# Kernel tuning notes

Hardware: AMD Instinct MI355X
Metric: run time of the kernel (lower is better)

## Reference

```python
import jax, jax.numpy as jnp
import numpy as np

B, T, C, H = 4, 4096, 512, 64

def setup_inputs() -> dict:
    key = jax.random.key(0)
    ks = jax.random.split(key, 9)
    k = jax.random.normal(ks[0], (B, T, C), dtype=jnp.float32)
    v = jax.random.normal(ks[1], (B, T, C), dtype=jnp.float32)
    q = jax.random.normal(ks[2], (B, T, C), dtype=jnp.float32)
    # causal lower-triangular mask, positions with 0 are masked to -inf
    mask = jnp.tril(jnp.ones((T, T), dtype=jnp.int32))
    s = 1.0 / np.sqrt(C)
    kW = jax.random.normal(ks[3], (C, H), dtype=jnp.float32) * s
    kb = jax.random.normal(ks[4], (H,), dtype=jnp.float32) * s
    vW = jax.random.normal(ks[5], (C, H), dtype=jnp.float32) * s
    vb = jax.random.normal(ks[6], (H,), dtype=jnp.float32) * s
    qW = jax.random.normal(ks[7], (C, H), dtype=jnp.float32) * s
    qb = jax.random.normal(ks[8], (H,), dtype=jnp.float32) * s
    return {"k": k, "v": v, "q": q, "mask": mask,
            "kW": kW, "kb": kb, "vW": vW, "vb": vb, "qW": qW, "qb": qb}

def reference(k, v, q, mask, kW, kb, vW, vb, qW, qb):
    C_in = k.shape[-1]
    kp = k @ kW + kb                              # [B,T,H]
    qp = q @ qW + qb                              # [B,T,H]
    # NOTE: original scales by embedding_size**-0.5 (C), not head_size**-0.5
    attn = jnp.einsum('bth,bsh->bts', qp, kp) * (C_in ** -0.5)  # [B,T,T]
    attn = jnp.where(mask[None, :, :] == 0, -jnp.inf, attn)
    attn = jax.nn.softmax(attn, axis=-1)
    vp = v @ vW + vb                              # [B,T,H]
    out = attn @ vp                               # [B,T,H]
    return out
```

## Files before the change

### kernel.cpp

```cpp
#include <hip/hip_runtime.h>
#include <hip/hip_bf16.h>

#define Bq 4
#define Tq 4096
#define Cq 512
#define Hq 64
#define NCH 8
#define CT 16
#define NEG_BIG (-3.0e38f)

using bf16   = __bf16;
using bf16x8 = __attribute__((ext_vector_type(8))) __bf16;
using bf16x4 = __attribute__((ext_vector_type(4))) __bf16;
using f32x4  = __attribute__((ext_vector_type(4))) float;
using f32x16 = __attribute__((ext_vector_type(16))) float;

static __device__ __forceinline__ float other_half_f(float x) {
    return __shfl_xor(x, 32, 64);
}
static __device__ __forceinline__ unsigned other_half_u(unsigned x) {
    return (unsigned)__shfl_xor((int)x, 32, 64);
}
static __device__ __forceinline__ unsigned pk2(float x, float y) {
    union { bf16 h[2]; unsigned u; } t;
    t.h[0] = (bf16)x; t.h[1] = (bf16)y;
    return t.u;
}
union W8 { unsigned u[4]; bf16x8 v; };

__global__ __launch_bounds__(256) void prep_weights_kernel(
    const float* __restrict__ kW, const float* __restrict__ qW,
    const float* __restrict__ vW, bf16* __restrict__ WT)
{
    int i = blockIdx.x * 256 + threadIdx.x;
    int t = i >> 15;
    int r = i & 32767;
    int h = r >> 9;
    int c = r & 511;
    const float* W = (t == 0) ? kW : (t == 1) ? qW : vW;
    WT[i] = (bf16)W[c * Hq + h];
}

__global__ __launch_bounds__(256) void proj_kernel(
    const float* __restrict__ Xk, const float* __restrict__ Xq,
    const float* __restrict__ Xv, const bf16* __restrict__ WT,
    const float* __restrict__ bk, const float* __restrict__ bq,
    const float* __restrict__ bv,
    bf16* __restrict__ kp, bf16* __restrict__ qp, bf16* __restrict__ vpT)
{
    const int t    = blockIdx.y;
    const int lane = threadIdx.x & 63;
    const int wave = threadIdx.x >> 6;
    const int lq   = lane & 15;
    const int lg   = lane >> 4;
    const int row0 = blockIdx.x * 64 + wave * 16;

    const float* X    = (t == 0) ? Xk : (t == 1) ? Xq : Xv;
    const float* bias = (t == 0) ? bk : (t == 1) ? bq : bv;
    const bf16*  Wt   = WT + (size_t)t * (Hq * Cq);

    const float* Xrow = X + (size_t)(row0 + lq) * Cq + lg * 8;

    f32x4 acc[4];
#pragma unroll
    for (int i = 0; i < 4; ++i) acc[i] = f32x4{0.f, 0.f, 0.f, 0.f};

#pragma unroll 4
    for (int kc = 0; kc < Cq; kc += 32) {
        float4 a0 = *(const float4*)(Xrow + kc);
        float4 a1 = *(const float4*)(Xrow + kc + 4);
        bf16x8 af;
        af[0] = (bf16)a0.x; af[1] = (bf16)a0.y; af[2] = (bf16)a0.z; af[3] = (bf16)a0.w;
        af[4] = (bf16)a1.x; af[5] = (bf16)a1.y; af[6] = (bf16)a1.z; af[7] = (bf16)a1.w;
#pragma unroll
        for (int ht = 0; ht < 4; ++ht) {
            bf16x8 bfB = *(const bf16x8*)(Wt + (size_t)(ht * 16 + lq) * Cq + kc + lg * 8);
            acc[ht] = __builtin_amdgcn_mfma_f32_16x16x32_bf16(af, bfB, acc[ht], 0, 0, 0);
        }
    }

    const float scale = (t == 1) ? 0.044194173824159216f : 1.0f;

    if (t < 2) {
        bf16* dst = (t == 0) ? kp : qp;
#pragma unroll
        for (int ht = 0; ht < 4; ++ht) {
            float bb = bias[ht * 16 + lq];
#pragma unroll
            for (int r = 0; r < 4; ++r) {
                int row = row0 + 4 * lg + r;
                dst[(size_t)row * Hq + ht * 16 + lq] = (bf16)((acc[ht][r] + bb) * scale);
            }
        }
    } else {
#pragma unroll
        for (int ht = 0; ht < 4; ++ht) {
            float bb = bias[ht * 16 + lq];
            bf16x4 pk;
#pragma unroll
            for (int r = 0; r < 4; ++r) pk[r] = (bf16)(acc[ht][r] + bb);
            int rowg = row0 + 4 * lg;
            int bidx = rowg >> 12;
            int tt   = rowg & 4095;
            int h    = ht * 16 + lq;
            *(bf16x4*)(vpT + (((size_t)(bidx * Hq + h)) << 12) + tt) = pk;
        }
    }
}

__global__ __launch_bounds__(64) void attn_kernel(
    const bf16* __restrict__ qp, const bf16* __restrict__ kp,
    const bf16* __restrict__ vpT,
    bf16* __restrict__ PO, float* __restrict__ PML)
{
    const int x = blockIdx.x;
    const int s = x & 7;
    const int b = s >> 1;
    const int a = ((x >> 3) << 1) | (s & 1);
    const int qb = a * 32;
    const int c = blockIdx.y;
    if (c * CT > a) return;

    const int lane = threadIdx.x;
    const int l31  = lane & 31;
    const int half = lane >> 5;
    const bool hi  = half != 0;

    const bf16* qrow = qp + ((size_t)b * Tq + qb + l31) * Hq + half * 8;
    const bf16x8 Q0 = *(const bf16x8*)(qrow);
    const bf16x8 Q1 = *(const bf16x8*)(qrow + 16);
    const bf16x8 Q2 = *(const bf16x8*)(qrow + 32);
    const bf16x8 Q3 = *(const bf16x8*)(qrow + 48);

    const bf16* Kb = kp  + (size_t)b * Tq * Hq;
    const bf16* Vb = vpT + (size_t)b * Hq * Tq;

    f32x16 O0, O1;
#pragma unroll
    for (int r = 0; r < 16; ++r) { O0[r] = 0.f; O1[r] = 0.f; }
    float m = NEG_BIG, l = 0.f;

    const int t0 = c * CT;
    const int t1 = min(a, t0 + CT - 1);

    for (int it = t0; it <= t1; ++it) {
        const int kb0 = it * 32;

        const bf16* kr = Kb + (size_t)(kb0 + l31) * Hq + half * 8;
        const bf16x8 K0 = *(const bf16x8*)(kr);
        const bf16x8 K1 = *(const bf16x8*)(kr + 16);
        const bf16x8 K2 = *(const bf16x8*)(kr + 32);
        const bf16x8 K3 = *(const bf16x8*)(kr + 48);
        const bf16* vr = Vb + (size_t)l31 * Tq + kb0 + half * 8;
        const bf16x8 V00 = *(const bf16x8*)(vr);
        const bf16x8 V01 = *(const bf16x8*)(vr + 16);
        const bf16x8 V10 = *(const bf16x8*)(vr + (size_t)32 * Tq);
        const bf16x8 V11 = *(const bf16x8*)(vr + (size_t)32 * Tq + 16);

        f32x16 S;
#pragma unroll
        for (int r = 0; r < 16; ++r) S[r] = 0.f;
        __builtin_amdgcn_s_setprio(1);
        S = __builtin_amdgcn_mfma_f32_32x32x16_bf16(K0, Q0, S, 0, 0, 0);
        S = __builtin_amdgcn_mfma_f32_32x32x16_bf16(K1, Q1, S, 0, 0, 0);
        S = __builtin_amdgcn_mfma_f32_32x32x16_bf16(K2, Q2, S, 0, 0, 0);
        S = __builtin_amdgcn_mfma_f32_32x32x16_bf16(K3, Q3, S, 0, 0, 0);
        __builtin_amdgcn_s_setprio(0);

        if (it == a) {
#pragma unroll
            for (int r = 0; r < 16; ++r) {
                const int kg = kb0 + (r & 3) + 8 * (r >> 2) + 4 * half;
                if (kg > qb + l31) S[r] = NEG_BIG;
            }
        }

        float tm = S[0];
#pragma unroll
        for (int r = 1; r < 16; ++r) tm = fmaxf(tm, S[r]);
        tm = fmaxf(tm, other_half_f(tm));
        const float mn   = fmaxf(m, tm);
        const float corr = __expf(m - mn);
        float p[16];
        float ps = 0.f;
#pragma unroll
        for (int r = 0; r < 16; ++r) { p[r] = __expf(S[r] - mn); ps += p[r]; }
        ps += other_half_f(ps);
        l = l * corr + ps;
        m = mn;
#pragma unroll
        for (int r = 0; r < 16; ++r) { O0[r] *= corr; O1[r] *= corr; }

        const unsigned w0 = pk2(p[0],  p[1]),  w1 = pk2(p[2],  p[3]);
        const unsigned w2 = pk2(p[4],  p[5]),  w3 = pk2(p[6],  p[7]);
        const unsigned w4 = pk2(p[8],  p[9]),  w5 = pk2(p[10], p[11]);
        const unsigned w6 = pk2(p[12], p[13]), w7 = pk2(p[14], p[15]);
        const unsigned o0 = other_half_u(w0), o1 = other_half_u(w1);
        const unsigned o2 = other_half_u(w2), o3 = other_half_u(w3);
        const unsigned o4 = other_half_u(w4), o5 = other_half_u(w5);
        const unsigned o6 = other_half_u(w6), o7 = other_half_u(w7);
        W8 B0, B1;
        B0.u[0] = hi ? o2 : w0;  B0.u[1] = hi ? o3 : w1;
        B0.u[2] = hi ? w2 : o0;  B0.u[3] = hi ? w3 : o1;
        B1.u[0] = hi ? o6 : w4;  B1.u[1] = hi ? o7 : w5;
        B1.u[2] = hi ? w6 : o4;  B1.u[3] = hi ? w7 : o5;

        __builtin_amdgcn_s_setprio(1);
        O0 = __builtin_amdgcn_mfma_f32_32x32x16_bf16(V00, B0.v, O0, 0, 0, 0);
        O0 = __builtin_amdgcn_mfma_f32_32x32x16_bf16(V01, B1.v, O0, 0, 0, 0);
        O1 = __builtin_amdgcn_mfma_f32_32x32x16_bf16(V10, B0.v, O1, 0, 0, 0);
        O1 = __builtin_amdgcn_mfma_f32_32x32x16_bf16(V11, B1.v, O1, 0, 0, 0);
        __builtin_amdgcn_s_setprio(0);
    }

    const float inv = 1.0f / l;
    const size_t slot = (size_t)(b * 128 + a) * NCH + c;
    bf16* po = PO + slot * 2048;
#pragma unroll
    for (int r = 0; r < 16; ++r) {
        const int h = (r & 3) + 8 * (r >> 2) + 4 * half;
        po[h * 32 + l31]        = (bf16)(O0[r] * inv);
        po[(h + 32) * 32 + l31] = (bf16)(O1[r] * inv);
    }
    if (half == 0) {
        PML[slot * 64 + l31]      = m;
        PML[slot * 64 + 32 + l31] = l;
    }
}

__global__ __launch_bounds__(256) void combine_kernel(
    const bf16* __restrict__ PO, const float* __restrict__ PML,
    float* __restrict__ out)
{
    const int gid = blockIdx.x;
    const int b   = gid & 3;
    const int a   = gid >> 2;
    const int qb  = a * 32;
    const int nch = (a >> 4) + 1;
    const int tid = threadIdx.x;
    const int q   = tid & 31;
    const int hh  = tid >> 5;
    const size_t slot0 = (size_t)(b * 128 + a) * NCH;

    float mx = NEG_BIG;
    for (int c = 0; c < nch; ++c)
        mx = fmaxf(mx, PML[(slot0 + c) * 64 + q]);

    float L = 0.f;
    float acc[8];
#pragma unroll
    for (int i = 0; i < 8; ++i) acc[i] = 0.f;

    for (int c = 0; c < nch; ++c) {
        const float mm = PML[(slot0 + c) * 64 + q];
        const float ll = PML[(slot0 + c) * 64 + 32 + q];
        const float w  = ll * __expf(mm - mx);
        L += w;
        const bf16* po = PO + (slot0 + c) * 2048;
#pragma unroll
        for (int ih = 0; ih < 8; ++ih)
            acc[ih] += w * (float)po[(hh + 8 * ih) * 32 + q];
    }
    const float inv = 1.0f / L;
#pragma unroll
    for (int ih = 0; ih < 8; ++ih)
        out[((size_t)b * Tq + qb + q) * Hq + hh + 8 * ih] = acc[ih] * inv;
}

extern "C" void kernel_launch(void* const* d_in, const int* in_sizes, int n_in,
                              void* d_out, int out_size, void* d_ws, size_t ws_size,
                              hipStream_t stream)
{
    const float* k  = (const float*)d_in[0];
    const float* v  = (const float*)d_in[1];
    const float* q  = (const float*)d_in[2];
    const float* kW = (const float*)d_in[4];
    const float* kb = (const float*)d_in[5];
    const float* vW = (const float*)d_in[6];
    const float* vb = (const float*)d_in[7];
    const float* qW = (const float*)d_in[8];
    const float* qb = (const float*)d_in[9];
    float* out = (float*)d_out;

    char* ws = (char*)d_ws;
    bf16*  WT  = (bf16*)(ws);
    bf16*  kp  = (bf16*)(ws + 196608);
    bf16*  qp  = (bf16*)(ws + 196608 + 2097152);
    bf16*  vpT = (bf16*)(ws + 196608 + 2 * 2097152);
    bf16*  PO  = (bf16*)(ws + 196608 + 3 * 2097152);
    float* PML = (float*)(ws + 196608 + 3 * 2097152 + 16777216);

    hipLaunchKernelGGL(prep_weights_kernel, dim3(384), dim3(256), 0, stream,
                       kW, qW, vW, WT);
    hipLaunchKernelGGL(proj_kernel, dim3(256, 3), dim3(256), 0, stream,
                       k, q, v, WT, kb, qb, vb, kp, qp, vpT);
    hipLaunchKernelGGL(attn_kernel, dim3(512, NCH), dim3(64), 0, stream,
                       qp, kp, vpT, PO, PML);
    hipLaunchKernelGGL(combine_kernel, dim3(512), dim3(256), 0, stream,
                       PO, PML, out);
}
```

Before: 99.76 us.

## Process 64-key tiles per iteration, split keys into 256-wide chunks, use exp2

```diff
diff --git a/kernel.cpp b/kernel.cpp
--- a/kernel.cpp
+++ b/kernel.cpp
@@ -5,8 +5,7 @@
 #define Tq 4096
 #define Cq 512
 #define Hq 64
-#define NCH 8
-#define CT 16
+#define NCH 16
 #define NEG_BIG (-3.0e38f)
 
 using bf16   = __bf16;
@@ -27,6 +26,30 @@
     return t.u;
 }
 union W8 { unsigned u[4]; bf16x8 v; };
+
+static __device__ __forceinline__ float max16(const f32x16& S) {
+    float a = fmaxf(S[0], S[1]),   b = fmaxf(S[2], S[3]);
+    float c = fmaxf(S[4], S[5]),   d = fmaxf(S[6], S[7]);
+    float e = fmaxf(S[8], S[9]),   f = fmaxf(S[10], S[11]);
+    float g = fmaxf(S[12], S[13]), h = fmaxf(S[14], S[15]);
+    return fmaxf(fmaxf(fmaxf(a, b), fmaxf(c, d)),
+                 fmaxf(fmaxf(e, f), fmaxf(g, h)));
+}
+
+#define BUILD_B(p, BA, BB) do {                                                \
+    const unsigned w0 = pk2(p[0],  p[1]),  w1 = pk2(p[2],  p[3]);              \
+    const unsigned w2 = pk2(p[4],  p[5]),  w3 = pk2(p[6],  p[7]);              \
+    const unsigned w4 = pk2(p[8],  p[9]),  w5 = pk2(p[10], p[11]);             \
+    const unsigned w6 = pk2(p[12], p[13]), w7 = pk2(p[14], p[15]);             \
+    const unsigned o0 = other_half_u(w0), o1 = other_half_u(w1);               \
+    const unsigned o2 = other_half_u(w2), o3 = other_half_u(w3);               \
+    const unsigned o4 = other_half_u(w4), o5 = other_half_u(w5);               \
+    const unsigned o6 = other_half_u(w6), o7 = other_half_u(w7);               \
+    BA.u[0] = hi ? o2 : w0;  BA.u[1] = hi ? o3 : w1;                           \
+    BA.u[2] = hi ? w2 : o0;  BA.u[3] = hi ? w3 : o1;                           \
+    BB.u[0] = hi ? o6 : w4;  BB.u[1] = hi ? o7 : w5;                           \
+    BB.u[2] = hi ? w6 : o4;  BB.u[3] = hi ? w7 : o5;                           \
+} while (0)
 
 __global__ __launch_bounds__(256) void prep_weights_kernel(
     const float* __restrict__ kW, const float* __restrict__ qW,
@@ -79,7 +102,7 @@
         }
     }
 
-    const float scale = (t == 1) ? 0.044194173824159216f : 1.0f;
+    const float scale = (t == 1) ? (0.044194173824159216f * 1.4426950408889634f) : 1.0f;
 
     if (t < 2) {
         bf16* dst = (t == 0) ? kp : qp;
@@ -113,18 +136,23 @@
     const bf16* __restrict__ vpT,
     bf16* __restrict__ PO, float* __restrict__ PML)
 {
-    const int x = blockIdx.x;
-    const int s = x & 7;
-    const int b = s >> 1;
-    const int a = ((x >> 3) << 1) | (s & 1);
+    const int x  = blockIdx.x;
+    const int s  = x & 7;
+    const int b  = s >> 1;
+    const int a  = ((x >> 3) << 1) | (s & 1);
     const int qb = a * 32;
-    const int c = blockIdx.y;
-    if (c * CT > a) return;
+    const int u  = a >> 3;
+    const int vv = a & 7;
+    const int c  = blockIdx.y;
+    if (c > u) return;
+    const int  nmac = (c < u) ? 4 : ((vv >> 1) + 1);
+    const bool diag = (c == u);
 
     const int lane = threadIdx.x;
     const int l31  = lane & 31;
     const int half = lane >> 5;
     const bool hi  = half != 0;
+    const int qg   = qb + l31;
 
     const bf16* qrow = qp + ((size_t)b * Tq + qb + l31) * Hq + half * 8;
     const bf16x8 Q0 = *(const bf16x8*)(qrow);
@@ -132,89 +160,99 @@
     const bf16x8 Q2 = *(const bf16x8*)(qrow + 32);
     const bf16x8 Q3 = *(const bf16x8*)(qrow + 48);
 
-    const bf16* Kb = kp  + (size_t)b * Tq * Hq;
-    const bf16* Vb = vpT + (size_t)b * Hq * Tq;
+    const bf16* Kb   = kp  + (size_t)b * Tq * Hq;
+    const bf16* vrow = vpT + (size_t)b * Hq * Tq + (size_t)l31 * Tq + half * 8;
 
     f32x16 O0, O1;
 #pragma unroll
     for (int r = 0; r < 16; ++r) { O0[r] = 0.f; O1[r] = 0.f; }
     float m = NEG_BIG, l = 0.f;
 
-    const int t0 = c * CT;
-    const int t1 = min(a, t0 + CT - 1);
-
-    for (int it = t0; it <= t1; ++it) {
-        const int kb0 = it * 32;
+    const int kbase = c * 256;
+    for (int mt = 0; mt < nmac; ++mt) {
+        const int kb0 = kbase + mt * 64;
 
         const bf16* kr = Kb + (size_t)(kb0 + l31) * Hq + half * 8;
-        const bf16x8 K0 = *(const bf16x8*)(kr);
-        const bf16x8 K1 = *(const bf16x8*)(kr + 16);
-        const bf16x8 K2 = *(const bf16x8*)(kr + 32);
-        const bf16x8 K3 = *(const bf16x8*)(kr + 48);
-        const bf16* vr = Vb + (size_t)l31 * Tq + kb0 + half * 8;
-        const bf16x8 V00 = *(const bf16x8*)(vr);
-        const bf16x8 V01 = *(const bf16x8*)(vr + 16);
-        const bf16x8 V10 = *(const bf16x8*)(vr + (size_t)32 * Tq);
-        const bf16x8 V11 = *(const bf16x8*)(vr + (size_t)32 * Tq + 16);
-
-        f32x16 S;
-#pragma unroll
-        for (int r = 0; r < 16; ++r) S[r] = 0.f;
+        const bf16x8 K00 = *(const bf16x8*)(kr);
+        const bf16x8 K01 = *(const bf16x8*)(kr + 16);
+        const bf16x8 K02 = *(const bf16x8*)(kr + 32);
+        const bf16x8 K03 = *(const bf16x8*)(kr + 48);
+        const bf16x8 K10 = *(const bf16x8*)(kr + 32 * Hq);
+        const bf16x8 K11 = *(const bf16x8*)(kr + 32 * Hq + 16);
+        const bf16x8 K12 = *(const bf16x8*)(kr + 32 * Hq + 32);
+        const bf16x8 K13 = *(const bf16x8*)(kr + 32 * Hq + 48);
+        const bf16* vr = vrow + kb0;
+        const bf16x8 Vh0k0 = *(const bf16x8*)(vr);
+        const bf16x8 Vh0k1 = *(const bf16x8*)(vr + 16);
+        const bf16x8 Vh0k2 = *(const bf16x8*)(vr + 32);
+        const bf16x8 Vh0k3 = *(const bf16x8*)(vr + 48);
+        const bf16x8 Vh1k0 = *(const bf16x8*)(vr + (size_t)32 * Tq);
+        const bf16x8 Vh1k1 = *(const bf16x8*)(vr + (size_t)32 * Tq + 16);
+        const bf16x8 Vh1k2 = *(const bf16x8*)(vr + (size_t)32 * Tq + 32);
+        const bf16x8 Vh1k3 = *(const bf16x8*)(vr + (size_t)32 * Tq + 48);
+
+        f32x16 S0, S1;
+#pragma unroll
+        for (int r = 0; r < 16; ++r) { S0[r] = 0.f; S1[r] = 0.f; }
         __builtin_amdgcn_s_setprio(1);
-        S = __builtin_amdgcn_mfma_f32_32x32x16_bf16(K0, Q0, S, 0, 0, 0);
-        S = __builtin_amdgcn_mfma_f32_32x32x16_bf16(K1, Q1, S, 0, 0, 0);
-        S = __builtin_amdgcn_mfma_f32_32x32x16_bf16(K2, Q2, S, 0, 0, 0);
-        S = __builtin_amdgcn_mfma_f32_32x32x16_bf16(K3, Q3, S, 0, 0, 0);
+        S0 = __builtin_amdgcn_mfma_f32_32x32x16_bf16(K00, Q0, S0, 0, 0, 0);
+        S1 = __builtin_amdgcn_mfma_f32_32x32x16_bf16(K10, Q0, S1, 0, 0, 0);
+        S0 = __builtin_amdgcn_mfma_f32_32x32x16_bf16(K01, Q1, S0, 0, 0, 0);
+        S1 = __builtin_amdgcn_mfma_f32_32x32x16_bf16(K11, Q1, S1, 0, 0, 0);
+        S0 = __builtin_amdgcn_mfma_f32_32x32x16_bf16(K02, Q2, S0, 0, 0, 0);
+        S1 = __builtin_amdgcn_mfma_f32_32x32x16_bf16(K12, Q2, S1, 0, 0, 0);
+        S0 = __builtin_amdgcn_mfma_f32_32x32x16_bf16(K03, Q3, S0, 0, 0, 0);
+        S1 = __builtin_amdgcn_mfma_f32_32x32x16_bf16(K13, Q3, S1, 0, 0, 0);
         __builtin_amdgcn_s_setprio(0);
 
-        if (it == a) {
+        if (diag) {
 #pragma unroll
             for (int r = 0; r < 16; ++r) {
                 const int kg = kb0 + (r & 3) + 8 * (r >> 2) + 4 * half;
-                if (kg > qb + l31) S[r] = NEG_BIG;
+                if (kg > qg)      S0[r] = NEG_BIG;
+                if (kg + 32 > qg) S1[r] = NEG_BIG;
             }
         }
 
-        float tm = S[0];
-#pragma unroll
-        for (int r = 1; r < 16; ++r) tm = fmaxf(tm, S[r]);
+        float tm = fmaxf(max16(S0), max16(S1));
         tm = fmaxf(tm, other_half_f(tm));
         const float mn   = fmaxf(m, tm);
-        const float corr = __expf(m - mn);
-        float p[16];
-        float ps = 0.f;
-#pragma unroll
-        for (int r = 0; r < 16; ++r) { p[r] = __expf(S[r] - mn); ps += p[r]; }
+        const float corr = exp2f(m - mn);
+        float p0[16], p1[16];
+#pragma unroll
+        for (int r = 0; r < 16; ++r) {
+            p0[r] = exp2f(S0[r] - mn);
+            p1[r] = exp2f(S1[r] - mn);
+        }
+        float ps = (((p0[0] + p0[1]) + (p0[2] + p0[3])) + ((p0[4] + p0[5]) + (p0[6] + p0[7])))
+                 + (((p0[8] + p0[9]) + (p0[10] + p0[11])) + ((p0[12] + p0[13]) + (p0[14] + p0[15])))
+                 + (((p1[0] + p1[1]) + (p1[2] + p1[3])) + ((p1[4] + p1[5]) + (p1[6] + p1[7])))
+                 + (((p1[8] + p1[9]) + (p1[10] + p1[11])) + ((p1[12] + p1[13]) + (p1[14] + p1[15])));
         ps += other_half_f(ps);
         l = l * corr + ps;
         m = mn;
 #pragma unroll
         for (int r = 0; r < 16; ++r) { O0[r] *= corr; O1[r] *= corr; }
 
-        const unsigned w0 = pk2(p[0],  p[1]),  w1 = pk2(p[2],  p[3]);
-        const unsigned w2 = pk2(p[4],  p[5]),  w3 = pk2(p[6],  p[7]);
-        const unsigned w4 = pk2(p[8],  p[9]),  w5 = pk2(p[10], p[11]);
-        const unsigned w6 = pk2(p[12], p[13]), w7 = pk2(p[14], p[15]);
-        const unsigned o0 = other_half_u(w0), o1 = other_half_u(w1);
-        const unsigned o2 = other_half_u(w2), o3 = other_half_u(w3);
-        const unsigned o4 = other_half_u(w4), o5 = other_half_u(w5);
-        const unsigned o6 = other_half_u(w6), o7 = other_half_u(w7);
-        W8 B0, B1;
-        B0.u[0] = hi ? o2 : w0;  B0.u[1] = hi ? o3 : w1;
-        B0.u[2] = hi ? w2 : o0;  B0.u[3] = hi ? w3 : o1;
-        B1.u[0] = hi ? o6 : w4;  B1.u[1] = hi ? o7 : w5;
-        B1.u[2] = hi ? w6 : o4;  B1.u[3] = hi ? w7 : o5;
+        W8 B00, B01, B10, B11;
+        BUILD_B(p0, B00, B01);
+        BUILD_B(p1, B10, B11);
 
         __builtin_amdgcn_s_setprio(1);
-        O0 = __builtin_amdgcn_mfma_f32_32x32x16_bf16(V00, B0.v, O0, 0, 0, 0);
-        O0 = __builtin_amdgcn_mfma_f32_32x32x16_bf16(V01, B1.v, O0, 0, 0, 0);
-        O1 = __builtin_amdgcn_mfma_f32_32x32x16_bf16(V10, B0.v, O1, 0, 0, 0);
-        O1 = __builtin_amdgcn_mfma_f32_32x32x16_bf16(V11, B1.v, O1, 0, 0, 0);
+        O0 = __builtin_amdgcn_mfma_f32_32x32x16_bf16(Vh0k0, B00.v, O0, 0, 0, 0);
+        O1 = __builtin_amdgcn_mfma_f32_32x32x16_bf16(Vh1k0, B00.v, O1, 0, 0, 0);
+        O0 = __builtin_amdgcn_mfma_f32_32x32x16_bf16(Vh0k1, B01.v, O0, 0, 0, 0);
+        O1 = __builtin_amdgcn_mfma_f32_32x32x16_bf16(Vh1k1, B01.v, O1, 0, 0, 0);
+        O0 = __builtin_amdgcn_mfma_f32_32x32x16_bf16(Vh0k2, B10.v, O0, 0, 0, 0);
+        O1 = __builtin_amdgcn_mfma_f32_32x32x16_bf16(Vh1k2, B10.v, O1, 0, 0, 0);
+        O0 = __builtin_amdgcn_mfma_f32_32x32x16_bf16(Vh0k3, B11.v, O0, 0, 0, 0);
+        O1 = __builtin_amdgcn_mfma_f32_32x32x16_bf16(Vh1k3, B11.v, O1, 0, 0, 0);
         __builtin_amdgcn_s_setprio(0);
     }
 
     const float inv = 1.0f / l;
-    const size_t slot = (size_t)(b * 128 + a) * NCH + c;
+    const int   sb   = b * 1088 + (u + 1) * ((u << 2) + vv);
+    const size_t slot = (size_t)sb + c;
     bf16* po = PO + slot * 2048;
 #pragma unroll
     for (int r = 0; r < 16; ++r) {
@@ -236,11 +274,12 @@
     const int b   = gid & 3;
     const int a   = gid >> 2;
     const int qb  = a * 32;
-    const int nch = (a >> 4) + 1;
+    const int u   = a >> 3, vv = a & 7;
+    const int nch = u + 1;
+    const size_t slot0 = (size_t)b * 1088 + (u + 1) * ((u << 2) + vv);
     const int tid = threadIdx.x;
     const int q   = tid & 31;
     const int hh  = tid >> 5;
-    const size_t slot0 = (size_t)(b * 128 + a) * NCH;
 
     float mx = NEG_BIG;
     for (int c = 0; c < nch; ++c)
@@ -254,7 +293,7 @@
     for (int c = 0; c < nch; ++c) {
         const float mm = PML[(slot0 + c) * 64 + q];
         const float ll = PML[(slot0 + c) * 64 + 32 + q];
-        const float w  = ll * __expf(mm - mx);
+        const float w  = ll * exp2f(mm - mx);
         L += w;
         const bf16* po = PO + (slot0 + c) * 2048;
 #pragma unroll
@@ -288,7 +327,7 @@
     bf16*  qp  = (bf16*)(ws + 196608 + 2097152);
     bf16*  vpT = (bf16*)(ws + 196608 + 2 * 2097152);
     bf16*  PO  = (bf16*)(ws + 196608 + 3 * 2097152);
-    float* PML = (float*)(ws + 196608 + 3 * 2097152 + 16777216);
+    float* PML = (float*)(ws + 196608 + 3 * 2097152 + 17825792);
 
     hipLaunchKernelGGL(prep_weights_kernel, dim3(384), dim3(256), 0, stream,
                        kW, qW, vW, WT);
```

Result: no change. 98.67 us (-1.1%).
